# Optimization experiments

Hardware: AMD Instinct MI355X
Metric: run time of the kernel (lower is better)

## Reference

```python
import jax, jax.numpy as jnp
import numpy as np

ALPHA = 2.0
EPS = 1e-12  # F.normalize default eps


def setup_inputs() -> dict:
    key = jax.random.key(0)
    k1, k2 = jax.random.split(key)
    x = jax.random.normal(k1, (16, 512, 48, 48), dtype=jnp.float32)
    # 1x1 conv weight [out=1, in=C, 1, 1] flattened to [C], xavier-like scale
    w_query = jax.random.normal(k2, (512,), dtype=jnp.float32) * (2.0 / (512 + 1)) ** 0.5
    return {"x": x, "w_query": w_query}


def reference(x, w_query):
    b, c, h, w = x.shape
    n = h * w
    # attention map from detached x: 1x1 conv (dot over channels) + softplus -> [b, n]
    xd = jax.lax.stop_gradient(x)
    att = jax.nn.softplus(jnp.einsum('bchw,c->bhw', xd, w_query)).reshape(b, n)
    # L2-normalize over channel dim, flatten spatial -> [b, c, n]
    norm = jnp.sqrt(jnp.sum(x * x, axis=1, keepdims=True))
    flat = (x / jnp.maximum(norm, EPS)).reshape(b, c, n)
    # full NxN similarity, relu^alpha
    sim = jnp.einsum('bcn,bcm->bnm', flat, flat)  # [b, n, n]
    score = jnp.maximum(sim, 0.0) ** ALPHA
    # combine with attention map -> refine score per spatial location
    refine = jnp.einsum('bnm,bm->bn', score, att).reshape(b, 1, h, w)
    # weighted global average pool -> [b, c, 1, 1]
    return jnp.mean(x * refine, axis=(2, 3), keepdims=True)
```

## Files before the change

### kernel.cpp

```cpp
#include <hip/hip_runtime.h>

#define C_DIM 512
#define N_PIX 2304
#define B_DIM 16
#define K8    (C_DIM / 8)
#define K8_STRIDE (N_PIX * 8)
#define FB_STRIDE ((size_t)K8 * K8_STRIDE)

typedef float floatx4 __attribute__((ext_vector_type(4)));
typedef __bf16 bf16x8 __attribute__((ext_vector_type(8)));

static __device__ __forceinline__ unsigned short f2bf(float f) {
    unsigned u = __float_as_uint(f);
    return (unsigned short)((u + 0x7fffu + ((u >> 16) & 1u)) >> 16);
}

static __device__ __forceinline__ float softplus_stable(float z) {
    return (z > 0.f) ? (z + log1pf(expf(-z))) : log1pf(expf(z));
}

static __device__ __forceinline__ void load_lds16(const void* gp, void* l) {
    __builtin_amdgcn_global_load_lds(
        (const __attribute__((address_space(1))) unsigned int*)gp,
        (__attribute__((address_space(3))) unsigned int*)l, 16, 0, 0);
}

__global__ __launch_bounds__(256) void xcvt_kernel(const float* __restrict__ x,
                                                   const float* __restrict__ w,
                                                   float* __restrict__ g,
                                                   float* __restrict__ rn2,
                                                   float* __restrict__ refine,
                                                   unsigned short* __restrict__ F) {
    const int tid = threadIdx.x;
    const int b  = (blockIdx.x * 64) / N_PIX;
    const int p0 = (blockIdx.x * 64) % N_PIX;
    const int n4l = tid & 15;
    const int k8b = tid >> 4;

    const float* xb = x + (size_t)b * C_DIM * N_PIX;
    float4 dot4 = {0.f, 0.f, 0.f, 0.f};
    float4 sq4  = {0.f, 0.f, 0.f, 0.f};

    #pragma unroll
    for (int it = 0; it < 4; ++it) {
        const int k8 = k8b + 16 * it;
        union { unsigned short u[4][8]; int4 v[4]; } cell;
        #pragma unroll
        for (int kk = 0; kk < 8; ++kk) {
            float4 xv = *(const float4*)(xb + (size_t)(k8 * 8 + kk) * N_PIX + p0 + n4l * 4);
            const float wc = w[k8 * 8 + kk];
            dot4.x = fmaf(xv.x, wc, dot4.x);  sq4.x = fmaf(xv.x, xv.x, sq4.x);
            dot4.y = fmaf(xv.y, wc, dot4.y);  sq4.y = fmaf(xv.y, xv.y, sq4.y);
            dot4.z = fmaf(xv.z, wc, dot4.z);  sq4.z = fmaf(xv.z, xv.z, sq4.z);
            dot4.w = fmaf(xv.w, wc, dot4.w);  sq4.w = fmaf(xv.w, xv.w, sq4.w);
            cell.u[0][kk] = f2bf(xv.x);
            cell.u[1][kk] = f2bf(xv.y);
            cell.u[2][kk] = f2bf(xv.z);
            cell.u[3][kk] = f2bf(xv.w);
        }
        unsigned short* dst = F + (size_t)b * FB_STRIDE + (size_t)k8 * K8_STRIDE
                            + (size_t)(p0 + n4l * 4) * 8;
        #pragma unroll
        for (int i = 0; i < 4; ++i)
            *(int4*)(dst + i * 8) = cell.v[i];
    }

    __shared__ float4 sdot[16][16];
    __shared__ float4 ssq[16][16];
    sdot[k8b][n4l] = dot4;
    ssq[k8b][n4l]  = sq4;
    __syncthreads();

    if (tid < 16) {
        float4 d = sdot[0][tid], s = ssq[0][tid];
        #pragma unroll
        for (int j = 1; j < 16; ++j) {
            float4 dj = sdot[j][tid], sj = ssq[j][tid];
            d.x += dj.x; d.y += dj.y; d.z += dj.z; d.w += dj.w;
            s.x += sj.x; s.y += sj.y; s.z += sj.z; s.w += sj.w;
        }
        float4 r2, gv;
        r2.x = 1.0f / fmaxf(s.x, 1e-24f);  gv.x = softplus_stable(d.x) * r2.x;
        r2.y = 1.0f / fmaxf(s.y, 1e-24f);  gv.y = softplus_stable(d.y) * r2.y;
        r2.z = 1.0f / fmaxf(s.z, 1e-24f);  gv.z = softplus_stable(d.z) * r2.z;
        r2.w = 1.0f / fmaxf(s.w, 1e-24f);  gv.w = softplus_stable(d.w) * r2.w;
        const int o = b * N_PIX + p0 + tid * 4;
        *(float4*)(g   + o) = gv;
        *(float4*)(rn2 + o) = r2;
        *(float4*)(refine + o) = (float4){0.f, 0.f, 0.f, 0.f};
    }
}

__global__ __launch_bounds__(256) void refine_kernel(const unsigned short* __restrict__ F,
                                                     const float* __restrict__ g,
                                                     float* __restrict__ refine) {
    const int id   = blockIdx.x;
    const int xcd  = id & 7;
    const int slot = id >> 3;
    const int hi   = (slot >= 171) ? 1 : 0;
    const int b    = xcd + 8 * hi;
    int t = slot - 171 * hi, bi = 0;
    while (t >= 18 - bi) { t -= 18 - bi; ++bi; }
    const int bj = bi + t;
    const int n0 = bi * 128;
    const int m0 = bj * 128;
    const bool mirror = (bi != bj);

    const unsigned short* Fb = F + (size_t)b * FB_STRIDE;
    const float* gb = g + b * N_PIX;

    __shared__ __align__(16) unsigned short As[8 * 128 * 8];
    __shared__ __align__(16) unsigned short Bs[8 * 128 * 8];

    const int tid  = threadIdx.x;
    const int lane = tid & 63;
    const int wave = tid >> 6;
    const int wr = wave >> 1, wc = wave & 1;
    const int quad = lane >> 4, lcol = lane & 15;

    floatx4 acc[4][4];
    #pragma unroll
    for (int i = 0; i < 4; ++i)
        #pragma unroll
        for (int j = 0; j < 4; ++j)
            acc[i][j] = (floatx4)0.f;

    const unsigned short* pA = Fb + (size_t)(wave * 2) * K8_STRIDE + (size_t)n0 * 8 + lane * 8;
    const unsigned short* pB = Fb + (size_t)(wave * 2) * K8_STRIDE + (size_t)m0 * 8 + lane * 8;
    unsigned short* const lA0 = &As[(wave * 2) * 1024];
    unsigned short* const lA1 = &As[(wave * 2 + 1) * 1024];
    unsigned short* const lB0 = &Bs[(wave * 2) * 1024];
    unsigned short* const lB1 = &Bs[(wave * 2 + 1) * 1024];

    for (int ck = 0; ck < 8; ++ck) {
        __syncthreads();
        load_lds16(pA,                    lA0);
        load_lds16(pA + 512,              lA0 + 512);
        load_lds16(pA + K8_STRIDE,        lA1);
        load_lds16(pA + K8_STRIDE + 512,  lA1 + 512);
        load_lds16(pB,                    lB0);
        load_lds16(pB + 512,              lB0 + 512);
        load_lds16(pB + K8_STRIDE,        lB1);
        load_lds16(pB + K8_STRIDE + 512,  lB1 + 512);
        pA += 8 * K8_STRIDE;
        pB += 8 * K8_STRIDE;
        __syncthreads();

        #pragma unroll
        for (int h = 0; h < 2; ++h) {
            const int kb = h * 4 + quad;
            bf16x8 af[4], bfr[4];
            #pragma unroll
            for (int mi = 0; mi < 4; ++mi)
                af[mi] = *(const bf16x8*)&As[(kb * 128 + wr * 64 + mi * 16 + lcol) * 8];
            #pragma unroll
            for (int ni = 0; ni < 4; ++ni)
                bfr[ni] = *(const bf16x8*)&Bs[(kb * 128 + wc * 64 + ni * 16 + lcol) * 8];
            #pragma unroll
            for (int mi = 0; mi < 4; ++mi)
                #pragma unroll
                for (int ni = 0; ni < 4; ++ni)
                    acc[mi][ni] = __builtin_amdgcn_mfma_f32_16x16x32_bf16(af[mi], bfr[ni], acc[mi][ni], 0, 0, 0);
        }
    }

    float gC[4];
    #pragma unroll
    for (int ni = 0; ni < 4; ++ni)
        gC[ni] = gb[m0 + wc * 64 + ni * 16 + lcol];

    #pragma unroll
    for (int mi = 0; mi < 4; ++mi) {
        float part[4] = {0.f, 0.f, 0.f, 0.f};
        #pragma unroll
        for (int ni = 0; ni < 4; ++ni) {
            #pragma unroll
            for (int r = 0; r < 4; ++r) {
                float s = fmaxf(acc[mi][ni][r], 0.f);
                part[r] = fmaf(s * s, gC[ni], part[r]);
            }
        }
        #pragma unroll
        for (int r = 0; r < 4; ++r) {
            float v = part[r];
            v += __shfl_xor(v, 1);
            v += __shfl_xor(v, 2);
            v += __shfl_xor(v, 4);
            v += __shfl_xor(v, 8);
            if (lcol == 0)
                atomicAdd(&refine[b * N_PIX + n0 + wr * 64 + mi * 16 + quad * 4 + r], v);
        }
    }

    if (mirror) {
        float gR[4][4];
        #pragma unroll
        for (int mi = 0; mi < 4; ++mi)
            #pragma unroll
            for (int r = 0; r < 4; ++r)
                gR[mi][r] = gb[n0 + wr * 64 + mi * 16 + quad * 4 + r];

        #pragma unroll
        for (int ni = 0; ni < 4; ++ni) {
            float msum = 0.f;
            #pragma unroll
            for (int mi = 0; mi < 4; ++mi) {
                #pragma unroll
                for (int r = 0; r < 4; ++r) {
                    float s = fmaxf(acc[mi][ni][r], 0.f);
                    msum = fmaf(s * s, gR[mi][r], msum);
                }
            }
            msum += __shfl_xor(msum, 16);
            msum += __shfl_xor(msum, 32);
            if (quad == 0)
                atomicAdd(&refine[b * N_PIX + m0 + wc * 64 + ni * 16 + lcol], msum);
        }
    }
}

__global__ __launch_bounds__(256) void pool_kernel(const unsigned short* __restrict__ F,
                                                   const float* __restrict__ refine,
                                                   const float* __restrict__ rn2,
                                                   float* __restrict__ out) {
    const int lane = threadIdx.x & 63;
    const int wave = threadIdx.x >> 6;
    const int b  = blockIdx.x >> 6;
    const int k8 = blockIdx.x & 63;
    const unsigned short* Fr = F + (size_t)b * FB_STRIDE + (size_t)k8 * K8_STRIDE;
    const float* rf = refine + b * N_PIX;
    const float* r2 = rn2 + b * N_PIX;
    float s[8] = {0.f, 0.f, 0.f, 0.f, 0.f, 0.f, 0.f, 0.f};
    #pragma unroll
    for (int j = 0; j < 9; ++j) {
        const int n = (j * 4 + wave) * 64 + lane;
        bf16x8 fv = *(const bf16x8*)(Fr + (size_t)n * 8);
        float rr = rf[n] * r2[n];
        #pragma unroll
        for (int kk = 0; kk < 8; ++kk)
            s[kk] = fmaf((float)fv[kk], rr, s[kk]);
    }
    __shared__ float sred[4][8];
    #pragma unroll
    for (int kk = 0; kk < 8; ++kk) {
        float v = s[kk];
        #pragma unroll
        for (int off = 32; off > 0; off >>= 1) v += __shfl_down(v, off);
        if (lane == 0) sred[wave][kk] = v;
    }
    __syncthreads();
    if (threadIdx.x < 8) {
        const int kk = threadIdx.x;
        out[b * C_DIM + k8 * 8 + kk] =
            (sred[0][kk] + sred[1][kk] + sred[2][kk] + sred[3][kk]) * (1.0f / N_PIX);
    }
}

__global__ __launch_bounds__(256) void prep_kernel(const float* __restrict__ x,
                                                   const float* __restrict__ w,
                                                   float* __restrict__ rnorm,
                                                   float* __restrict__ att) {
    const int tid = threadIdx.x;
    const int px = tid & 63;
    const int cc = tid >> 6;
    const int pglob = blockIdx.x * 64 + px;
    const int b = pglob / N_PIX;
    const int p = pglob - b * N_PIX;

    const float* xb = x + (size_t)b * C_DIM * N_PIX + p;
    float dot = 0.f, sq = 0.f;
    #pragma unroll 4
    for (int c = cc * 128; c < cc * 128 + 128; ++c) {
        float v = xb[(size_t)c * N_PIX];
        dot = fmaf(v, w[c], dot);
        sq  = fmaf(v, v, sq);
    }
    __shared__ float sdot[4][64];
    __shared__ float ssq[4][64];
    sdot[cc][px] = dot;
    ssq[cc][px]  = sq;
    __syncthreads();
    if (cc == 0) {
        dot = sdot[0][px] + sdot[1][px] + sdot[2][px] + sdot[3][px];
        sq  = ssq[0][px]  + ssq[1][px]  + ssq[2][px]  + ssq[3][px];
        att[pglob] = softplus_stable(dot);
        rnorm[pglob] = 1.0f / fmaxf(sqrtf(sq), 1e-12f);
    }
}

__global__ __launch_bounds__(256) void refine_fallback(const float* __restrict__ x,
                                                       const float* __restrict__ rnorm,
                                                       const float* __restrict__ att,
                                                       float* __restrict__ refine) {
    const int b  = blockIdx.z;
    const int n0 = blockIdx.x * 128;
    const int m0 = blockIdx.y * 128;
    const float* xb = x + (size_t)b * C_DIM * N_PIX;
    const float* rn = rnorm + b * N_PIX;
    const float* ab = att + b * N_PIX;

    __shared__ __align__(16) unsigned short As[4 * 128 * 8];
    __shared__ __align__(16) unsigned short Bs[4 * 128 * 8];

    const int tid  = threadIdx.x;
    const int nl   = tid & 127;
    const int half = tid >> 7;
    const int lane = tid & 63;
    const int wave = tid >> 6;
    const int wr = wave >> 1, wc = wave & 1;
    const int quad = lane >> 4, lcol = lane & 15;

    const float rA = rn[n0 + nl];
    const float rB = rn[m0 + nl];

    floatx4 acc[4][4];
    #pragma unroll
    for (int i = 0; i < 4; ++i)
        #pragma unroll
        for (int j = 0; j < 4; ++j)
            acc[i][j] = (floatx4)0.f;

    for (int k0 = 0; k0 < C_DIM; k0 += 32) {
        const float* xa = xb + (size_t)(k0 + half * 16) * N_PIX;
        union { unsigned short u[16]; int4 v[2]; } ta, tb;
        #pragma unroll
        for (int j = 0; j < 16; ++j) {
            float va = xa[(size_t)j * N_PIX + n0 + nl];
            float vb = xa[(size_t)j * N_PIX + m0 + nl];
            ta.u[j] = f2bf(va * rA);
            tb.u[j] = f2bf(vb * rB);
        }
        __syncthreads();
        *(int4*)&As[((half * 2 + 0) * 128 + nl) * 8] = ta.v[0];
        *(int4*)&As[((half * 2 + 1) * 128 + nl) * 8] = ta.v[1];
        *(int4*)&Bs[((half * 2 + 0) * 128 + nl) * 8] = tb.v[0];
        *(int4*)&Bs[((half * 2 + 1) * 128 + nl) * 8] = tb.v[1];
        __syncthreads();

        bf16x8 af[4], bfr[4];
        #pragma unroll
        for (int mi = 0; mi < 4; ++mi)
            af[mi] = *(const bf16x8*)&As[(quad * 128 + wr * 64 + mi * 16 + lcol) * 8];
        #pragma unroll
        for (int ni = 0; ni < 4; ++ni)
            bfr[ni] = *(const bf16x8*)&Bs[(quad * 128 + wc * 64 + ni * 16 + lcol) * 8];
        #pragma unroll
        for (int mi = 0; mi < 4; ++mi)
            #pragma unroll
            for (int ni = 0; ni < 4; ++ni)
                acc[mi][ni] = __builtin_amdgcn_mfma_f32_16x16x32_bf16(af[mi], bfr[ni], acc[mi][ni], 0, 0, 0);
    }

    float attv[4];
    #pragma unroll
    for (int ni = 0; ni < 4; ++ni)
        attv[ni] = ab[m0 + wc * 64 + ni * 16 + lcol];

    #pragma unroll
    for (int mi = 0; mi < 4; ++mi) {
        float part[4] = {0.f, 0.f, 0.f, 0.f};
        #pragma unroll
        for (int ni = 0; ni < 4; ++ni) {
            #pragma unroll
            for (int r = 0; r < 4; ++r) {
                float s = fmaxf(acc[mi][ni][r], 0.f);
                part[r] = fmaf(s * s, attv[ni], part[r]);
            }
        }
        #pragma unroll
        for (int r = 0; r < 4; ++r) {
            float v = part[r];
            v += __shfl_xor(v, 1);
            v += __shfl_xor(v, 2);
            v += __shfl_xor(v, 4);
            v += __shfl_xor(v, 8);
            if (lcol == 0)
                atomicAdd(&refine[b * N_PIX + n0 + wr * 64 + mi * 16 + quad * 4 + r], v);
        }
    }
}

__global__ __launch_bounds__(256) void pool_fallback(const float* __restrict__ x,
                                                     const float* __restrict__ refine,
                                                     float* __restrict__ out) {
    const int lane = threadIdx.x & 63;
    const int wave = threadIdx.x >> 6;
    const int gidx = blockIdx.x * 4 + wave;
    const int b = gidx >> 9;
    const float4* xr = (const float4*)(x + (size_t)gidx * N_PIX);
    const float4* rr = (const float4*)(refine + (size_t)b * N_PIX);
    float s = 0.f;
    #pragma unroll
    for (int j = 0; j < 9; ++j) {
        float4 xv = xr[j * 64 + lane];
        float4 rv = rr[j * 64 + lane];
        s += xv.x * rv.x + xv.y * rv.y + xv.z * rv.z + xv.w * rv.w;
    }
    #pragma unroll
    for (int off = 32; off > 0; off >>= 1) s += __shfl_down(s, off);
    if (lane == 0) out[gidx] = s * (1.0f / N_PIX);
}

extern "C" void kernel_launch(void* const* d_in, const int* in_sizes, int n_in,
                              void* d_out, int out_size, void* d_ws, size_t ws_size,
                              hipStream_t stream) {
    const float* x = (const float*)d_in[0];
    const float* w = (const float*)d_in[1];
    float* rn2    = (float*)d_ws;
    float* g      = rn2 + B_DIM * N_PIX;
    float* refine = g + B_DIM * N_PIX;
    unsigned short* F = (unsigned short*)(refine + B_DIM * N_PIX);
    float* out    = (float*)d_out;

    const size_t need = (size_t)3 * B_DIM * N_PIX * 4 + (size_t)B_DIM * FB_STRIDE * 2;

    if (ws_size >= need) {
        xcvt_kernel<<<dim3(B_DIM * N_PIX / 64), 256, 0, stream>>>(x, w, g, rn2, refine, F);
        refine_kernel<<<dim3(171 * 16), 256, 0, stream>>>(F, g, refine);
        pool_kernel<<<dim3(B_DIM * K8), 256, 0, stream>>>(F, refine, rn2, out);
    } else {
        hipMemsetAsync(refine, 0, B_DIM * N_PIX * sizeof(float), stream);
        prep_kernel<<<dim3(B_DIM * N_PIX / 64), 256, 0, stream>>>(x, w, rn2, g);
        refine_fallback<<<dim3(18, 18, B_DIM), 256, 0, stream>>>(x, rn2, g, refine);
        pool_fallback<<<dim3(B_DIM * C_DIM / 4), 256, 0, stream>>>(x, refine, out);
    }
}
```

Before: 208.7 us.

## Split conversion over channel groups with atomics and shrink refine LDS tile

```diff
diff --git a/kernel.cpp b/kernel.cpp
--- a/kernel.cpp
+++ b/kernel.cpp
@@ -6,6 +6,7 @@
 #define K8    (C_DIM / 8)
 #define K8_STRIDE (N_PIX * 8)
 #define FB_STRIDE ((size_t)K8 * K8_STRIDE)
+#define NB (B_DIM * N_PIX)
 
 typedef float floatx4 __attribute__((ext_vector_type(4)));
 typedef __bf16 bf16x8 __attribute__((ext_vector_type(8)));
@@ -27,68 +28,48 @@
 
 __global__ __launch_bounds__(256) void xcvt_kernel(const float* __restrict__ x,
                                                    const float* __restrict__ w,
-                                                   float* __restrict__ g,
-                                                   float* __restrict__ rn2,
-                                                   float* __restrict__ refine,
-                                                   unsigned short* __restrict__ F) {
-    const int tid = threadIdx.x;
-    const int b  = (blockIdx.x * 64) / N_PIX;
-    const int p0 = (blockIdx.x * 64) % N_PIX;
-    const int n4l = tid & 15;
-    const int k8b = tid >> 4;
-
-    const float* xb = x + (size_t)b * C_DIM * N_PIX;
-    float4 dot4 = {0.f, 0.f, 0.f, 0.f};
-    float4 sq4  = {0.f, 0.f, 0.f, 0.f};
-
-    #pragma unroll
-    for (int it = 0; it < 4; ++it) {
-        const int k8 = k8b + 16 * it;
-        union { unsigned short u[4][8]; int4 v[4]; } cell;
+                                                   unsigned short* __restrict__ F,
+                                                   float* __restrict__ accd,
+                                                   float* __restrict__ accs) {
+    const int pg = blockIdx.x;
+    const int cg = blockIdx.y;
+    const int b  = pg / 9;
+    const int p  = (pg - b * 9) * 256 + threadIdx.x;
+    const float* xb = x + (size_t)b * C_DIM * N_PIX + p;
+
+    float dot = 0.f, sq = 0.f;
+    #pragma unroll
+    for (int k8l = 0; k8l < 4; ++k8l) {
+        const int k8 = cg * 4 + k8l;
+        float v[8];
+        #pragma unroll
+        for (int kk = 0; kk < 8; ++kk)
+            v[kk] = xb[(size_t)(k8 * 8 + kk) * N_PIX];
+        union { unsigned short u[8]; int4 q; } cell;
         #pragma unroll
         for (int kk = 0; kk < 8; ++kk) {
-            float4 xv = *(const float4*)(xb + (size_t)(k8 * 8 + kk) * N_PIX + p0 + n4l * 4);
-            const float wc = w[k8 * 8 + kk];
-            dot4.x = fmaf(xv.x, wc, dot4.x);  sq4.x = fmaf(xv.x, xv.x, sq4.x);
-            dot4.y = fmaf(xv.y, wc, dot4.y);  sq4.y = fmaf(xv.y, xv.y, sq4.y);
-            dot4.z = fmaf(xv.z, wc, dot4.z);  sq4.z = fmaf(xv.z, xv.z, sq4.z);
-            dot4.w = fmaf(xv.w, wc, dot4.w);  sq4.w = fmaf(xv.w, xv.w, sq4.w);
-            cell.u[0][kk] = f2bf(xv.x);
-            cell.u[1][kk] = f2bf(xv.y);
-            cell.u[2][kk] = f2bf(xv.z);
-            cell.u[3][kk] = f2bf(xv.w);
-        }
-        unsigned short* dst = F + (size_t)b * FB_STRIDE + (size_t)k8 * K8_STRIDE
-                            + (size_t)(p0 + n4l * 4) * 8;
-        #pragma unroll
-        for (int i = 0; i < 4; ++i)
-            *(int4*)(dst + i * 8) = cell.v[i];
-    }
-
-    __shared__ float4 sdot[16][16];
-    __shared__ float4 ssq[16][16];
-    sdot[k8b][n4l] = dot4;
-    ssq[k8b][n4l]  = sq4;
-    __syncthreads();
-
-    if (tid < 16) {
-        float4 d = sdot[0][tid], s = ssq[0][tid];
-        #pragma unroll
-        for (int j = 1; j < 16; ++j) {
-            float4 dj = sdot[j][tid], sj = ssq[j][tid];
-            d.x += dj.x; d.y += dj.y; d.z += dj.z; d.w += dj.w;
-            s.x += sj.x; s.y += sj.y; s.z += sj.z; s.w += sj.w;
-        }
-        float4 r2, gv;
-        r2.x = 1.0f / fmaxf(s.x, 1e-24f);  gv.x = softplus_stable(d.x) * r2.x;
-        r2.y = 1.0f / fmaxf(s.y, 1e-24f);  gv.y = softplus_stable(d.y) * r2.y;
-        r2.z = 1.0f / fmaxf(s.z, 1e-24f);  gv.z = softplus_stable(d.z) * r2.z;
-        r2.w = 1.0f / fmaxf(s.w, 1e-24f);  gv.w = softplus_stable(d.w) * r2.w;
-        const int o = b * N_PIX + p0 + tid * 4;
-        *(float4*)(g   + o) = gv;
-        *(float4*)(rn2 + o) = r2;
-        *(float4*)(refine + o) = (float4){0.f, 0.f, 0.f, 0.f};
-    }
+            dot = fmaf(v[kk], w[k8 * 8 + kk], dot);
+            sq  = fmaf(v[kk], v[kk], sq);
+            cell.u[kk] = f2bf(v[kk]);
+        }
+        *(int4*)(F + (size_t)b * FB_STRIDE + (size_t)k8 * K8_STRIDE + (size_t)p * 8) = cell.q;
+    }
+    atomicAdd(&accd[b * N_PIX + p], dot);
+    atomicAdd(&accs[b * N_PIX + p], sq);
+}
+
+__global__ __launch_bounds__(256) void finalize_kernel(const float* __restrict__ accd,
+                                                       const float* __restrict__ accs,
+                                                       float* __restrict__ g,
+                                                       float* __restrict__ rn2,
+                                                       float* __restrict__ refine) {
+    const int bp = blockIdx.x * 256 + threadIdx.x;
+    const float d = accd[bp];
+    const float s = accs[bp];
+    const float r2 = 1.0f / fmaxf(s, 1e-24f);
+    g[bp]      = softplus_stable(d) * r2;
+    rn2[bp]    = r2;
+    refine[bp] = 0.f;
 }
 
 __global__ __launch_bounds__(256) void refine_kernel(const unsigned short* __restrict__ F,
@@ -109,8 +90,8 @@
     const unsigned short* Fb = F + (size_t)b * FB_STRIDE;
     const float* gb = g + b * N_PIX;
 
-    __shared__ __align__(16) unsigned short As[8 * 128 * 8];
-    __shared__ __align__(16) unsigned short Bs[8 * 128 * 8];
+    __shared__ __align__(16) unsigned short As[4 * 128 * 8];
+    __shared__ __align__(16) unsigned short Bs[4 * 128 * 8];
 
     const int tid  = threadIdx.x;
     const int lane = tid & 63;
@@ -125,43 +106,31 @@
         for (int j = 0; j < 4; ++j)
             acc[i][j] = (floatx4)0.f;
 
-    const unsigned short* pA = Fb + (size_t)(wave * 2) * K8_STRIDE + (size_t)n0 * 8 + lane * 8;
-    const unsigned short* pB = Fb + (size_t)(wave * 2) * K8_STRIDE + (size_t)m0 * 8 + lane * 8;
-    unsigned short* const lA0 = &As[(wave * 2) * 1024];
-    unsigned short* const lA1 = &As[(wave * 2 + 1) * 1024];
-    unsigned short* const lB0 = &Bs[(wave * 2) * 1024];
-    unsigned short* const lB1 = &Bs[(wave * 2 + 1) * 1024];
-
-    for (int ck = 0; ck < 8; ++ck) {
+    const unsigned short* gA = Fb + (size_t)wave * K8_STRIDE + (size_t)n0 * 8 + lane * 8;
+    const unsigned short* gB = Fb + (size_t)wave * K8_STRIDE + (size_t)m0 * 8 + lane * 8;
+
+    for (int ck = 0; ck < 16; ++ck) {
+        const unsigned short* sA = gA + (size_t)ck * (4 * K8_STRIDE);
+        const unsigned short* sB = gB + (size_t)ck * (4 * K8_STRIDE);
         __syncthreads();
-        load_lds16(pA,                    lA0);
-        load_lds16(pA + 512,              lA0 + 512);
-        load_lds16(pA + K8_STRIDE,        lA1);
-        load_lds16(pA + K8_STRIDE + 512,  lA1 + 512);
-        load_lds16(pB,                    lB0);
-        load_lds16(pB + 512,              lB0 + 512);
-        load_lds16(pB + K8_STRIDE,        lB1);
-        load_lds16(pB + K8_STRIDE + 512,  lB1 + 512);
-        pA += 8 * K8_STRIDE;
-        pB += 8 * K8_STRIDE;
+        load_lds16(sA,       &As[wave * 1024]);
+        load_lds16(sA + 512, &As[wave * 1024 + 512]);
+        load_lds16(sB,       &Bs[wave * 1024]);
+        load_lds16(sB + 512, &Bs[wave * 1024 + 512]);
         __syncthreads();
 
-        #pragma unroll
-        for (int h = 0; h < 2; ++h) {
-            const int kb = h * 4 + quad;
-            bf16x8 af[4], bfr[4];
-            #pragma unroll
-            for (int mi = 0; mi < 4; ++mi)
-                af[mi] = *(const bf16x8*)&As[(kb * 128 + wr * 64 + mi * 16 + lcol) * 8];
+        bf16x8 af[4], bfr[4];
+        #pragma unroll
+        for (int mi = 0; mi < 4; ++mi)
+            af[mi] = *(const bf16x8*)&As[(quad * 128 + wr * 64 + mi * 16 + lcol) * 8];
+        #pragma unroll
+        for (int ni = 0; ni < 4; ++ni)
+            bfr[ni] = *(const bf16x8*)&Bs[(quad * 128 + wc * 64 + ni * 16 + lcol) * 8];
+        #pragma unroll
+        for (int mi = 0; mi < 4; ++mi)
             #pragma unroll
             for (int ni = 0; ni < 4; ++ni)
-                bfr[ni] = *(const bf16x8*)&Bs[(kb * 128 + wc * 64 + ni * 16 + lcol) * 8];
-            #pragma unroll
-            for (int mi = 0; mi < 4; ++mi)
-                #pragma unroll
-                for (int ni = 0; ni < 4; ++ni)
-                    acc[mi][ni] = __builtin_amdgcn_mfma_f32_16x16x32_bf16(af[mi], bfr[ni], acc[mi][ni], 0, 0, 0);
-        }
+                acc[mi][ni] = __builtin_amdgcn_mfma_f32_16x16x32_bf16(af[mi], bfr[ni], acc[mi][ni], 0, 0, 0);
     }
 
     float gC[4];
@@ -407,20 +376,24 @@
     const float* x = (const float*)d_in[0];
     const float* w = (const float*)d_in[1];
     float* rn2    = (float*)d_ws;
-    float* g      = rn2 + B_DIM * N_PIX;
-    float* refine = g + B_DIM * N_PIX;
-    unsigned short* F = (unsigned short*)(refine + B_DIM * N_PIX);
+    float* g      = rn2 + NB;
+    float* refine = g + NB;
+    float* accd   = refine + NB;
+    float* accs   = accd + NB;
+    unsigned short* F = (unsigned short*)(accs + NB);
     float* out    = (float*)d_out;
 
-    const size_t need = (size_t)3 * B_DIM * N_PIX * 4 + (size_t)B_DIM * FB_STRIDE * 2;
+    const size_t need = (size_t)5 * NB * 4 + (size_t)B_DIM * FB_STRIDE * 2;
 
     if (ws_size >= need) {
-        xcvt_kernel<<<dim3(B_DIM * N_PIX / 64), 256, 0, stream>>>(x, w, g, rn2, refine, F);
+        hipMemsetAsync(accd, 0, (size_t)2 * NB * 4, stream);
+        xcvt_kernel<<<dim3(144, 16), 256, 0, stream>>>(x, w, F, accd, accs);
+        finalize_kernel<<<dim3(144), 256, 0, stream>>>(accd, accs, g, rn2, refine);
         refine_kernel<<<dim3(171 * 16), 256, 0, stream>>>(F, g, refine);
         pool_kernel<<<dim3(B_DIM * K8), 256, 0, stream>>>(F, refine, rn2, out);
     } else {
-        hipMemsetAsync(refine, 0, B_DIM * N_PIX * sizeof(float), stream);
-        prep_kernel<<<dim3(B_DIM * N_PIX / 64), 256, 0, stream>>>(x, w, rn2, g);
+        hipMemsetAsync(refine, 0, (size_t)NB * 4, stream);
+        prep_kernel<<<dim3(NB / 64), 256, 0, stream>>>(x, w, rn2, g);
         refine_fallback<<<dim3(18, 18, B_DIM), 256, 0, stream>>>(x, rn2, g, refine);
         pool_fallback<<<dim3(B_DIM * C_DIM / 4), 256, 0, stream>>>(x, refine, out);
     }
```

Result: faster. 183.5 us (-12.1%).
